# Performance work log

Hardware: AMD Instinct MI355X
Metric: run time of the kernel (lower is better)

Reference implementation:

```python
import jax, jax.numpy as jnp
import numpy as np

B, N, D_IN, D_HID, D_OUT = 8192, 32, 512, 512, 512


def setup_inputs() -> dict:
    key = jax.random.key(0)
    ks = jax.random.split(key, 5)
    scale_mlp = (6.0 / (D_IN + D_HID)) ** 0.5
    scale_out = (6.0 / (D_HID + D_OUT)) ** 0.5
    return {
        "self_vecs": jax.random.normal(ks[0], (B, D_IN), dtype=jnp.float32),
        "neigh_vecs": jax.random.normal(ks[1], (B, N, D_IN), dtype=jnp.float32),
        "mlp_w": jax.random.uniform(ks[2], (D_IN, D_HID), jnp.float32, -scale_mlp, scale_mlp),
        "mlp_b": jnp.zeros((D_HID,), dtype=jnp.float32),
        "neigh_w": jax.random.uniform(ks[3], (D_HID, D_OUT), jnp.float32, -scale_out, scale_out),
        "self_w": jax.random.uniform(ks[4], (D_IN, D_OUT), jnp.float32, -scale_out, scale_out),
    }


def reference(self_vecs, neigh_vecs, mlp_w, mlp_b, neigh_w, self_w):
    # per-neighbor MLP: [B,N,D_in] @ [D_in,D_hid] + b, relu (dropout=0)
    h = jax.nn.relu(jnp.einsum('bni,ih->bnh', neigh_vecs, mlp_w) + mlp_b)
    # max-pool over neighbors -> [B, D_hid]
    pooled = jnp.max(h, axis=1)
    from_neighs = pooled @ neigh_w          # [B, D_out]
    from_self = self_vecs @ self_w          # [B, D_out]
    return jax.nn.relu(from_self + from_neighs)
```

## Files before the change

### kernel.cpp

```cpp
#include <hip/hip_runtime.h>
#include <hip/hip_bf16.h>
#include <stdint.h>

#define D 512

typedef __attribute__((ext_vector_type(8))) short short8_t;
typedef __attribute__((ext_vector_type(4))) float floatx4;

static __device__ __forceinline__ unsigned short f2bf(float f) {
    union { __hip_bfloat16 h; unsigned short u; } c;
    c.h = __float2bfloat16(f);
    return c.u;
}

__global__ void __launch_bounds__(256) prep_weights(
    const float* __restrict__ w1, const float* __restrict__ w2,
    const float* __restrict__ w3,
    unsigned short* __restrict__ w1t, unsigned short* __restrict__ w2t,
    unsigned short* __restrict__ w3t)
{
    int idx = blockIdx.x * 256 + threadIdx.x;
    int m = idx >> 18;
    int i = idx & 262143;
    int k = i >> 9, n = i & 511;
    const float* src = (m == 0) ? w1 : (m == 1) ? w2 : w3;
    unsigned short* dst = (m == 0) ? w1t : (m == 1) ? w2t : w3t;
    dst[n * D + k] = f2bf(src[i]);
}

__global__ void __launch_bounds__(256) mlp_pool_kernel(
    const float* __restrict__ neigh,
    const unsigned short* __restrict__ w1t,
    const float* __restrict__ bias,
    unsigned short* __restrict__ pooled)
{
    __shared__ __align__(16) short As[128 * 64];
    __shared__ __align__(16) short Bs[128 * 64];
    __shared__ float pool_s[4][128];

    const int tid  = threadIdx.x;
    const int wave = tid >> 6;
    const int lane = tid & 63;
    const int quad = lane >> 4;
    const int l15  = lane & 15;
    const int mw = (wave >> 1) * 64;
    const int nw = (wave & 1) * 64;

    const int m0 = (blockIdx.x >> 2) * 128;
    const int n0 = (blockIdx.x & 3) * 128;

    floatx4 acc[4][4];
#pragma unroll
    for (int i = 0; i < 4; ++i)
#pragma unroll
        for (int j = 0; j < 4; ++j) acc[i][j] = (floatx4){0.f, 0.f, 0.f, 0.f};

    for (int kk = 0; kk < 8; ++kk) {
        const int k0 = kk * 64;
        __syncthreads();
#pragma unroll
        for (int rnd = 0; rnd < 4; ++rnd) {
            int l = rnd * 256 + tid;
            int r = l >> 3, g = l & 7;
            const float4* src = reinterpret_cast<const float4*>(
                neigh + (size_t)(m0 + r) * D + k0 + g * 8);
            float4 f0 = src[0];
            float4 f1 = src[1];
            short8_t v;
            v[0] = (short)f2bf(f0.x); v[1] = (short)f2bf(f0.y);
            v[2] = (short)f2bf(f0.z); v[3] = (short)f2bf(f0.w);
            v[4] = (short)f2bf(f1.x); v[5] = (short)f2bf(f1.y);
            v[6] = (short)f2bf(f1.z); v[7] = (short)f2bf(f1.w);
            *reinterpret_cast<short8_t*>(&As[r * 64 + ((g ^ (r & 7)) * 8)]) = v;
        }
#pragma unroll
        for (int rnd = 0; rnd < 4; ++rnd) {
            int l = rnd * 256 + tid;
            int r = l >> 3, g = l & 7;
            short8_t v = *reinterpret_cast<const short8_t*>(
                w1t + (size_t)(n0 + r) * D + k0 + g * 8);
            *reinterpret_cast<short8_t*>(&Bs[r * 64 + ((g ^ (r & 7)) * 8)]) = v;
        }
        __syncthreads();
#pragma unroll
        for (int s = 0; s < 2; ++s) {
            short8_t af[4], bfr[4];
#pragma unroll
            for (int mt = 0; mt < 4; ++mt) {
                int r = mw + mt * 16 + l15;
                int c = (s * 4 + quad) ^ (r & 7);
                af[mt] = *reinterpret_cast<const short8_t*>(&As[r * 64 + c * 8]);
            }
#pragma unroll
            for (int nt = 0; nt < 4; ++nt) {
                int r = nw + nt * 16 + l15;
                int c = (s * 4 + quad) ^ (r & 7);
                bfr[nt] = *reinterpret_cast<const short8_t*>(&Bs[r * 64 + c * 8]);
            }
#pragma unroll
            for (int mt = 0; mt < 4; ++mt)
#pragma unroll
                for (int nt = 0; nt < 4; ++nt)
                    acc[mt][nt] = __builtin_amdgcn_mfma_f32_16x16x32_bf16(
                        af[mt], bfr[nt], acc[mt][nt], 0, 0, 0);
        }
    }

#pragma unroll
    for (int gl = 0; gl < 2; ++gl) {
#pragma unroll
        for (int nt = 0; nt < 4; ++nt) {
            float v = -3.4e38f;
#pragma unroll
            for (int mt = 2 * gl; mt < 2 * gl + 2; ++mt)
#pragma unroll
                for (int rg = 0; rg < 4; ++rg) v = fmaxf(v, acc[mt][nt][rg]);
            v = fmaxf(v, __shfl_xor(v, 16));
            v = fmaxf(v, __shfl_xor(v, 32));
            if (lane < 16) pool_s[(mw >> 5) + gl][nw + nt * 16 + l15] = v;
        }
    }
    __syncthreads();
    for (int i = tid; i < 512; i += 256) {
        int g = i >> 7, col = i & 127;
        float v = fmaxf(pool_s[g][col] + bias[n0 + col], 0.0f);
        pooled[(size_t)((m0 >> 5) + g) * D + n0 + col] = f2bf(v);
    }
}

__global__ void __launch_bounds__(256) out_gemm_kernel(
    const unsigned short* __restrict__ pooled,
    const float* __restrict__ selfv,
    const unsigned short* __restrict__ w2t,
    const unsigned short* __restrict__ w3t,
    float* __restrict__ out)
{
    __shared__ __align__(16) short As[128 * 64];
    __shared__ __align__(16) short Bs[128 * 64];

    const int tid  = threadIdx.x;
    const int wave = tid >> 6;
    const int lane = tid & 63;
    const int quad = lane >> 4;
    const int l15  = lane & 15;
    const int mw = (wave >> 1) * 64;
    const int nw = (wave & 1) * 64;

    const int m0 = (blockIdx.x >> 2) * 128;
    const int n0 = (blockIdx.x & 3) * 128;

    floatx4 acc[4][4];
#pragma unroll
    for (int i = 0; i < 4; ++i)
#pragma unroll
        for (int j = 0; j < 4; ++j) acc[i][j] = (floatx4){0.f, 0.f, 0.f, 0.f};

    for (int kk = 0; kk < 16; ++kk) {
        const int k0 = (kk & 7) * 64;
        __syncthreads();
        if (kk < 8) {
#pragma unroll
            for (int rnd = 0; rnd < 4; ++rnd) {
                int l = rnd * 256 + tid;
                int r = l >> 3, g = l & 7;
                short8_t v = *reinterpret_cast<const short8_t*>(
                    pooled + (size_t)(m0 + r) * D + k0 + g * 8);
                *reinterpret_cast<short8_t*>(&As[r * 64 + ((g ^ (r & 7)) * 8)]) = v;
            }
#pragma unroll
            for (int rnd = 0; rnd < 4; ++rnd) {
                int l = rnd * 256 + tid;
                int r = l >> 3, g = l & 7;
                short8_t v = *reinterpret_cast<const short8_t*>(
                    w2t + (size_t)(n0 + r) * D + k0 + g * 8);
                *reinterpret_cast<short8_t*>(&Bs[r * 64 + ((g ^ (r & 7)) * 8)]) = v;
            }
        } else {
#pragma unroll
            for (int rnd = 0; rnd < 4; ++rnd) {
                int l = rnd * 256 + tid;
                int r = l >> 3, g = l & 7;
                const float4* src = reinterpret_cast<const float4*>(
                    selfv + (size_t)(m0 + r) * D + k0 + g * 8);
                float4 f0 = src[0];
                float4 f1 = src[1];
                short8_t v;
                v[0] = (short)f2bf(f0.x); v[1] = (short)f2bf(f0.y);
                v[2] = (short)f2bf(f0.z); v[3] = (short)f2bf(f0.w);
                v[4] = (short)f2bf(f1.x); v[5] = (short)f2bf(f1.y);
                v[6] = (short)f2bf(f1.z); v[7] = (short)f2bf(f1.w);
                *reinterpret_cast<short8_t*>(&As[r * 64 + ((g ^ (r & 7)) * 8)]) = v;
            }
#pragma unroll
            for (int rnd = 0; rnd < 4; ++rnd) {
                int l = rnd * 256 + tid;
                int r = l >> 3, g = l & 7;
                short8_t v = *reinterpret_cast<const short8_t*>(
                    w3t + (size_t)(n0 + r) * D + k0 + g * 8);
                *reinterpret_cast<short8_t*>(&Bs[r * 64 + ((g ^ (r & 7)) * 8)]) = v;
            }
        }
        __syncthreads();
#pragma unroll
        for (int s = 0; s < 2; ++s) {
            short8_t af[4], bfr[4];
#pragma unroll
            for (int mt = 0; mt < 4; ++mt) {
                int r = mw + mt * 16 + l15;
                int c = (s * 4 + quad) ^ (r & 7);
                af[mt] = *reinterpret_cast<const short8_t*>(&As[r * 64 + c * 8]);
            }
#pragma unroll
            for (int nt = 0; nt < 4; ++nt) {
                int r = nw + nt * 16 + l15;
                int c = (s * 4 + quad) ^ (r & 7);
                bfr[nt] = *reinterpret_cast<const short8_t*>(&Bs[r * 64 + c * 8]);
            }
#pragma unroll
            for (int mt = 0; mt < 4; ++mt)
#pragma unroll
                for (int nt = 0; nt < 4; ++nt)
                    acc[mt][nt] = __builtin_amdgcn_mfma_f32_16x16x32_bf16(
                        af[mt], bfr[nt], acc[mt][nt], 0, 0, 0);
        }
    }

#pragma unroll
    for (int mt = 0; mt < 4; ++mt)
#pragma unroll
        for (int nt = 0; nt < 4; ++nt)
#pragma unroll
            for (int rg = 0; rg < 4; ++rg) {
                int row = m0 + mw + mt * 16 + quad * 4 + rg;
                int col = n0 + nw + nt * 16 + l15;
                out[(size_t)row * D + col] = fmaxf(acc[mt][nt][rg], 0.0f);
            }
}

extern "C" void kernel_launch(void* const* d_in, const int* in_sizes, int n_in,
                              void* d_out, int out_size, void* d_ws, size_t ws_size,
                              hipStream_t stream) {
    const float* selfv = (const float*)d_in[0];
    const float* neigh = (const float*)d_in[1];
    const float* w1    = (const float*)d_in[2];
    const float* b1    = (const float*)d_in[3];
    const float* w2    = (const float*)d_in[4];
    const float* w3    = (const float*)d_in[5];
    float* out = (float*)d_out;

    unsigned short* pooled = (unsigned short*)d_ws;
    unsigned short* w1t = (unsigned short*)((char*)d_ws + 8388608);
    unsigned short* w2t = w1t + 262144;
    unsigned short* w3t = w2t + 262144;

    prep_weights<<<3072, 256, 0, stream>>>(w1, w2, w3, w1t, w2t, w3t);
    mlp_pool_kernel<<<8192, 256, 0, stream>>>(neigh, w1t, b1, pooled);
    out_gemm_kernel<<<256, 256, 0, stream>>>(pooled, selfv, w2t, w3t, out);
}
```

Baseline: 913.9 us.

## Use direct global-to-LDS loads and retile MLP-pool GEMM to 64x256

The MLP+maxpool GEMM kernel now stages the fp32 neighbor tile and bf16 weight tile straight into LDS with global_load_lds, so the data no longer passes through registers. The fp32 to bf16 conversion moves to the point where A fragments are read from LDS. The block tile changes from 128x128 to 64x256 with per-wave 32x128, and the swizzle is reworked to match. The aim is to cut VGPR staging traffic and to read each neighbor row fewer times across N-blocks (2 instead of 4), at the cost of repeating the conversion per wave and a larger LDS footprint.

```diff
diff --git a/kernel.cpp b/kernel.cpp
--- a/kernel.cpp
+++ b/kernel.cpp
@@ -11,6 +11,12 @@
     union { __hip_bfloat16 h; unsigned short u; } c;
     c.h = __float2bfloat16(f);
     return c.u;
+}
+
+static __device__ __forceinline__ void ld_lds16(const void* g, void* l) {
+    __builtin_amdgcn_global_load_lds(
+        (const __attribute__((address_space(1))) void*)g,
+        (__attribute__((address_space(3))) void*)l, 16, 0, 0);
 }
 
 __global__ void __launch_bounds__(256) prep_weights(
@@ -34,95 +40,100 @@
     const float* __restrict__ bias,
     unsigned short* __restrict__ pooled)
 {
-    __shared__ __align__(16) short As[128 * 64];
-    __shared__ __align__(16) short Bs[128 * 64];
-    __shared__ float pool_s[4][128];
+    __shared__ __align__(16) float As[64 * 64];
+    __shared__ __align__(16) short Bs[256 * 64];
+    __shared__ float pool_s[2][256];
 
     const int tid  = threadIdx.x;
     const int wave = tid >> 6;
     const int lane = tid & 63;
     const int quad = lane >> 4;
     const int l15  = lane & 15;
-    const int mw = (wave >> 1) * 64;
-    const int nw = (wave & 1) * 64;
-
-    const int m0 = (blockIdx.x >> 2) * 128;
-    const int n0 = (blockIdx.x & 3) * 128;
-
-    floatx4 acc[4][4];
-#pragma unroll
-    for (int i = 0; i < 4; ++i)
-#pragma unroll
-        for (int j = 0; j < 4; ++j) acc[i][j] = (floatx4){0.f, 0.f, 0.f, 0.f};
+    const int mw = (wave >> 1) * 32;
+    const int nw = (wave & 1) * 128;
+
+    const int m0 = (blockIdx.x >> 1) * 64;
+    const int n0 = (blockIdx.x & 1) * 256;
+
+    const float* agp[4];
+#pragma unroll
+    for (int rr = 0; rr < 4; ++rr) {
+        int ci = wave * 256 + rr * 64 + lane;
+        int r = ci >> 4, pos = ci & 15, ch = pos ^ (r & 15);
+        agp[rr] = neigh + (size_t)(m0 + r) * D + ch * 4;
+    }
+    char* alp0 = (char*)As + wave * 4096 + lane * 16;
+    const unsigned short* bgp0 = w1t +
+        (size_t)(n0 + wave * 64 + (lane >> 3)) * D +
+        ((lane & 7) ^ ((lane >> 3) & 7)) * 8;
+    char* blp0 = (char*)Bs + wave * 8192 + lane * 16;
+
+    floatx4 acc[2][8];
+#pragma unroll
+    for (int i = 0; i < 2; ++i)
+#pragma unroll
+        for (int j = 0; j < 8; ++j) acc[i][j] = (floatx4){0.f, 0.f, 0.f, 0.f};
 
     for (int kk = 0; kk < 8; ++kk) {
         const int k0 = kk * 64;
         __syncthreads();
 #pragma unroll
-        for (int rnd = 0; rnd < 4; ++rnd) {
-            int l = rnd * 256 + tid;
-            int r = l >> 3, g = l & 7;
-            const float4* src = reinterpret_cast<const float4*>(
-                neigh + (size_t)(m0 + r) * D + k0 + g * 8);
-            float4 f0 = src[0];
-            float4 f1 = src[1];
-            short8_t v;
-            v[0] = (short)f2bf(f0.x); v[1] = (short)f2bf(f0.y);
-            v[2] = (short)f2bf(f0.z); v[3] = (short)f2bf(f0.w);
-            v[4] = (short)f2bf(f1.x); v[5] = (short)f2bf(f1.y);
-            v[6] = (short)f2bf(f1.z); v[7] = (short)f2bf(f1.w);
-            *reinterpret_cast<short8_t*>(&As[r * 64 + ((g ^ (r & 7)) * 8)]) = v;
+        for (int rr = 0; rr < 4; ++rr)
+            ld_lds16(agp[rr] + k0, alp0 + rr * 1024);
+#pragma unroll
+        for (int rr = 0; rr < 8; ++rr)
+            ld_lds16(bgp0 + rr * 4096 + k0, blp0 + rr * 1024);
+        __syncthreads();
+
+#pragma unroll
+        for (int s = 0; s < 2; ++s) {
+            short8_t af[2], bf[8];
+#pragma unroll
+            for (int mt = 0; mt < 2; ++mt) {
+                int r = mw + mt * 16 + l15;
+                int c2 = s * 8 + quad * 2;
+                floatx4 a0 = *(const floatx4*)(
+                    (const char*)As + r * 256 + ((c2 ^ l15) * 16));
+                floatx4 a1 = *(const floatx4*)(
+                    (const char*)As + r * 256 + (((c2 + 1) ^ l15) * 16));
+                short8_t v;
+                v[0] = (short)f2bf(a0[0]); v[1] = (short)f2bf(a0[1]);
+                v[2] = (short)f2bf(a0[2]); v[3] = (short)f2bf(a0[3]);
+                v[4] = (short)f2bf(a1[0]); v[5] = (short)f2bf(a1[1]);
+                v[6] = (short)f2bf(a1[2]); v[7] = (short)f2bf(a1[3]);
+                af[mt] = v;
+            }
+#pragma unroll
+            for (int nt = 0; nt < 8; ++nt) {
+                int r = nw + nt * 16 + l15;
+                int c = (s * 4 + quad) ^ (l15 & 7);
+                bf[nt] = *(const short8_t*)((const char*)Bs + r * 128 + c * 16);
+            }
+#pragma unroll
+            for (int mt = 0; mt < 2; ++mt)
+#pragma unroll
+                for (int nt = 0; nt < 8; ++nt)
+                    acc[mt][nt] = __builtin_amdgcn_mfma_f32_16x16x32_bf16(
+                        af[mt], bf[nt], acc[mt][nt], 0, 0, 0);
         }
-#pragma unroll
-        for (int rnd = 0; rnd < 4; ++rnd) {
-            int l = rnd * 256 + tid;
-            int r = l >> 3, g = l & 7;
-            short8_t v = *reinterpret_cast<const short8_t*>(
-                w1t + (size_t)(n0 + r) * D + k0 + g * 8);
-            *reinterpret_cast<short8_t*>(&Bs[r * 64 + ((g ^ (r & 7)) * 8)]) = v;
-        }
-        __syncthreads();
-#pragma unroll
-        for (int s = 0; s < 2; ++s) {
-            short8_t af[4], bfr[4];
-#pragma unroll
-            for (int mt = 0; mt < 4; ++mt) {
-                int r = mw + mt * 16 + l15;
-                int c = (s * 4 + quad) ^ (r & 7);
-                af[mt] = *reinterpret_cast<const short8_t*>(&As[r * 64 + c * 8]);
-            }
-#pragma unroll
-            for (int nt = 0; nt < 4; ++nt) {
-                int r = nw + nt * 16 + l15;
-                int c = (s * 4 + quad) ^ (r & 7);
-                bfr[nt] = *reinterpret_cast<const short8_t*>(&Bs[r * 64 + c * 8]);
-            }
-#pragma unroll
-            for (int mt = 0; mt < 4; ++mt)
-#pragma unroll
-                for (int nt = 0; nt < 4; ++nt)
-                    acc[mt][nt] = __builtin_amdgcn_mfma_f32_16x16x32_bf16(
-                        af[mt], bfr[nt], acc[mt][nt], 0, 0, 0);
-        }
-    }
-
-#pragma unroll
-    for (int gl = 0; gl < 2; ++gl) {
-#pragma unroll
-        for (int nt = 0; nt < 4; ++nt) {
-            float v = -3.4e38f;
-#pragma unroll
-            for (int mt = 2 * gl; mt < 2 * gl + 2; ++mt)
-#pragma unroll
-                for (int rg = 0; rg < 4; ++rg) v = fmaxf(v, acc[mt][nt][rg]);
-            v = fmaxf(v, __shfl_xor(v, 16));
-            v = fmaxf(v, __shfl_xor(v, 32));
-            if (lane < 16) pool_s[(mw >> 5) + gl][nw + nt * 16 + l15] = v;
-        }
+    }
+
+#pragma unroll
+    for (int nt = 0; nt < 8; ++nt) {
+        float v = -3.4e38f;
+#pragma unroll
+        for (int mt = 0; mt < 2; ++mt)
+#pragma unroll
+            for (int rg = 0; rg < 4; ++rg) v = fmaxf(v, acc[mt][nt][rg]);
+        v = fmaxf(v, __shfl_xor(v, 16));
+        v = fmaxf(v, __shfl_xor(v, 32));
+        if (lane < 16) pool_s[wave >> 1][nw + nt * 16 + l15] = v;
     }
     __syncthreads();
-    for (int i = tid; i < 512; i += 256) {
-        int g = i >> 7, col = i & 127;
+#pragma unroll
+    for (int it = 0; it < 2; ++it) {
+        int i = it * 256 + tid;
+        int g = i >> 8, col = i & 255;
         float v = fmaxf(pool_s[g][col] + bias[n0 + col], 0.0f);
         pooled[(size_t)((m0 >> 5) + g) * D + n0 + col] = f2bf(v);
     }
```

After: 836.0 us. -8.5%, faster.
